# Kernel optimization log

Hardware: AMD Instinct MI355X
Metric: run time of the kernel (lower is better)

The kernel has to match this reference:

```python
import jax, jax.numpy as jnp
import numpy as np

NEG_SLOPE = 0.2


def gat_conv(h, src, dst, n_dst, W_src, W_dst, attn_l, attn_r, bias):
    # h: [N_src, F_in]; edges src->dst; dst nodes are a prefix of src nodes.
    H, D = attn_l.shape
    z_src = (h @ W_src).reshape(h.shape[0], H, D)          # [N_src, H, D]
    z_dst = (h[:n_dst] @ W_dst).reshape(n_dst, H, D)       # [N_dst, H, D]
    el = jnp.einsum('nhd,hd->nh', z_src, attn_l)           # [N_src, H]
    er = jnp.einsum('nhd,hd->nh', z_dst, attn_r)           # [N_dst, H]
    e = jax.nn.leaky_relu(el[src] + er[dst], NEG_SLOPE)    # [E, H]
    # numerically stable edge softmax over incoming edges of each dst node
    m = jax.ops.segment_max(e, dst, num_segments=n_dst)    # [N_dst, H]
    w = jnp.exp(e - m[dst])                                # [E, H]
    s = jax.ops.segment_sum(w, dst, num_segments=n_dst)    # [N_dst, H]
    alpha = w / s[dst]                                     # [E, H]
    msg = alpha[:, :, None] * z_src[src]                   # [E, H, D]
    out = jax.ops.segment_sum(msg, dst, num_segments=n_dst)
    return out + bias                                      # [N_dst, H, D]


def setup_inputs() -> dict:
    key = jax.random.key(0)
    ks = jax.random.split(key, 16)
    IN, HID, HEADS, NCLS = 256, 64, 4, 47
    N_SRC0, N_DST0, E0 = 200000, 50000, 500000
    N_DST1, E1 = 10000, 100000
    sc0 = 0.1
    inp = {
        'x': jax.random.normal(ks[0], (N_SRC0, IN), jnp.float32),
        'src0': jax.random.randint(ks[1], (E0,), 0, N_SRC0, jnp.int32),
        'dst0': jax.random.randint(ks[2], (E0,), 0, N_DST0, jnp.int32),
        'src1': jax.random.randint(ks[3], (E1,), 0, N_DST0, jnp.int32),
        'dst1': jax.random.randint(ks[4], (E1,), 0, N_DST1, jnp.int32),
        'num_dst0': N_DST0,
        'num_dst1': N_DST1,
        'W0_src': jax.random.normal(ks[5], (IN, HEADS * HID), jnp.float32) * sc0,
        'W0_dst': jax.random.normal(ks[6], (IN, HEADS * HID), jnp.float32) * sc0,
        'attn_l0': jax.random.normal(ks[7], (HEADS, HID), jnp.float32) * sc0,
        'attn_r0': jax.random.normal(ks[8], (HEADS, HID), jnp.float32) * sc0,
        'bias0': jnp.zeros((HEADS, HID), jnp.float32),
        'W1_src': jax.random.normal(ks[9], (HEADS * HID, HEADS * NCLS), jnp.float32) * sc0,
        'W1_dst': jax.random.normal(ks[10], (HEADS * HID, HEADS * NCLS), jnp.float32) * sc0,
        'attn_l1': jax.random.normal(ks[11], (HEADS, NCLS), jnp.float32) * sc0,
        'attn_r1': jax.random.normal(ks[12], (HEADS, NCLS), jnp.float32) * sc0,
        'bias1': jnp.zeros((HEADS, NCLS), jnp.float32),
    }
    return inp


def reference(x, src0, dst0, src1, dst1, num_dst0, num_dst1,
              W0_src, W0_dst, attn_l0, attn_r0, bias0,
              W1_src, W1_dst, attn_l1, attn_r1, bias1):
    # layer 0: GATConv + relu activation, flatten heads
    h = gat_conv(x, src0, dst0, num_dst0, W0_src, W0_dst, attn_l0, attn_r0, bias0)
    h = jax.nn.relu(h).reshape(num_dst0, -1)               # [N_dst0, H*HID]
    # layer 1: GATConv, no activation
    h = gat_conv(h, src1, dst1, num_dst1, W1_src, W1_dst, attn_l1, attn_r1, bias1)
    h = h.mean(axis=1)                                     # mean over heads -> [N_dst1, n_classes]
    return jax.nn.log_softmax(h, axis=-1)
```

## Files before the change

kernel.cpp:

```cpp
#include <hip/hip_runtime.h>
#include <math.h>

typedef _Float16 half8 __attribute__((ext_vector_type(8)));
typedef _Float16 half4 __attribute__((ext_vector_type(4)));
typedef float f32x4 __attribute__((ext_vector_type(4)));

constexpr int IN    = 256;
constexpr int NCLS  = 47;
constexpr int HD1   = 188;
constexpr float NEG_SLOPE = 0.2f;
constexpr int ND0 = 50000, ND1 = 10000;

static __device__ __forceinline__ float leaky(float x) {
    return x >= 0.f ? x : NEG_SLOPE * x;
}

__device__ __forceinline__ void gload16(const void* g, void* l) {
    __builtin_amdgcn_global_load_lds((const __attribute__((address_space(1))) void*)g,
                                     (__attribute__((address_space(3))) void*)l, 16, 0, 0);
}

__device__ __forceinline__ float red8(const float v[8], int lane) {
    const int b0 = lane & 1, b1 = (lane >> 1) & 1, b2 = (lane >> 2) & 1;
    float K[4];
#pragma unroll
    for (int i = 0; i < 4; ++i) {
        float send = b0 ? v[i] : v[i + 4];
        float r = __shfl_xor(send, 1);
        K[i] = (b0 ? v[i + 4] : v[i]) + r;
    }
    float L[2];
#pragma unroll
    for (int i = 0; i < 2; ++i) {
        float send = b1 ? K[i] : K[i + 2];
        float r = __shfl_xor(send, 2);
        L[i] = (b1 ? K[i + 2] : K[i]) + r;
    }
    float send = b2 ? L[0] : L[1];
    float r = __shfl_xor(send, 4);
    float Mv = (b2 ? L[1] : L[0]) + r;
    Mv += __shfl_xor(Mv, 8);
    Mv += __shfl_xor(Mv, 16);
    Mv += __shfl_xor(Mv, 32);
    return Mv;
}

__global__ __launch_bounds__(256) void prep_k(
        const float* __restrict__ W0s, const float* __restrict__ W1s,
        const float* __restrict__ W0d, const float* __restrict__ W1d,
        const float* __restrict__ al0, const float* __restrict__ ar0,
        const float* __restrict__ al1, const float* __restrict__ ar1,
        _Float16* __restrict__ B0p, _Float16* __restrict__ B1p,
        float* __restrict__ vl0T, float* __restrict__ vr0T,
        float* __restrict__ vl1T, float* __restrict__ vr1T) {
    int b = blockIdx.x, t = threadIdx.x;
    if (b < 256) {
        int id = b * 256 + t;
        int h = id >> 14, n = (id >> 8) & 63, k = id & 255;
        int dst = (h * 64 + n) * 256 + ((((k >> 3) ^ (n & 31)) & 31) << 3) + (k & 7);
        B0p[dst] = (_Float16)W0s[(size_t)k * 256 + h * 64 + n];
    } else if (b < 448) {
        int id = (b - 256) * 256 + t;
        int np = id >> 8, k = id & 255;
        int h = np / 48, n = np % 48;
        int dst = np * 256 + ((((k >> 3) ^ (n & 31)) & 31) << 3) + (k & 7);
        B1p[dst] = (n < NCLS) ? (_Float16)W1s[(size_t)k * HD1 + h * NCLS + n] : (_Float16)0.f;
    } else if (b == 448) {
        for (int i = t; i < 1024; i += 256) {
            int h = i >> 8, k = i & 255;
            float s = 0.f;
            for (int d = 0; d < 64; ++d)
                s += W0d[(size_t)k * 256 + h * 64 + d] * ar0[h * 64 + d];
            vr0T[h * 256 + k] = s;
        }
    } else if (b == 449) {
        for (int i = t; i < 1024; i += 256) {
            int h = i >> 8, k = i & 255;
            float s = 0.f;
            for (int d = 0; d < 64; ++d)
                s += W0s[(size_t)k * 256 + h * 64 + d] * al0[h * 64 + d];
            vl0T[h * 256 + k] = s;
        }
    } else if (b == 450) {
        for (int i = t; i < 1024; i += 256) {
            int h = i >> 8, k = i & 255;
            float s = 0.f;
            for (int d = 0; d < NCLS; ++d)
                s += W1s[(size_t)k * HD1 + h * NCLS + d] * al1[h * NCLS + d];
            vl1T[h * 256 + k] = s;
        }
    } else {
        for (int i = t; i < 1024; i += 256) {
            int h = i >> 8, k = i & 255;
            float s = 0.f;
            for (int d = 0; d < NCLS; ++d)
                s += W1d[(size_t)k * HD1 + h * NCLS + d] * ar1[h * NCLS + d];
            vr1T[h * 256 + k] = s;
        }
    }
}

template <bool F32IN, bool WRITE_XH>
__global__ __launch_bounds__(256) void lr_k(const void* __restrict__ Xv,
        const float* __restrict__ vlT, const float* __restrict__ vrT,
        _Float16* __restrict__ xh, float* __restrict__ el, float* __restrict__ er,
        int M, int Mr) {
    const int wv = threadIdx.x >> 6, lane = threadIdx.x & 63;
    const int gw0 = blockIdx.x * 4 + wv, NW = gridDim.x * 4;
    float vl[4][4], vr[4][4];
#pragma unroll
    for (int h = 0; h < 4; ++h) {
        float4 v = *(const float4*)(vlT + h * 256 + lane * 4);
        vl[h][0] = v.x; vl[h][1] = v.y; vl[h][2] = v.z; vl[h][3] = v.w;
        float4 u = *(const float4*)(vrT + h * 256 + lane * 4);
        vr[h][0] = u.x; vr[h][1] = u.y; vr[h][2] = u.z; vr[h][3] = u.w;
    }
    const int l7 = lane & 7;
    const int jj = ((l7 >> 1) & 1) * 2 + ((l7 >> 2) & 1);
    const bool isL = (l7 & 1) == 0;

    auto dorow = [&](int row) {
        float xa[4];
        if constexpr (F32IN) {
            float4 tv = *(const float4*)((const float*)Xv + (size_t)row * 256 + lane * 4);
            xa[0] = tv.x; xa[1] = tv.y; xa[2] = tv.z; xa[3] = tv.w;
            if constexpr (WRITE_XH) {
                half4 hv;
                hv[0] = (_Float16)tv.x; hv[1] = (_Float16)tv.y;
                hv[2] = (_Float16)tv.z; hv[3] = (_Float16)tv.w;
                *(half4*)(xh + (size_t)row * 256 + lane * 4) = hv;
            }
        } else {
            half4 tv = *(const half4*)((const _Float16*)Xv + (size_t)row * 256 + lane * 4);
            xa[0] = (float)tv[0]; xa[1] = (float)tv[1];
            xa[2] = (float)tv[2]; xa[3] = (float)tv[3];
        }
        float v8[8];
#pragma unroll
        for (int h = 0; h < 4; ++h) {
            v8[h]     = xa[0] * vl[h][0] + xa[1] * vl[h][1]
                      + xa[2] * vl[h][2] + xa[3] * vl[h][3];
            v8[h + 4] = xa[0] * vr[h][0] + xa[1] * vr[h][1]
                      + xa[2] * vr[h][2] + xa[3] * vr[h][3];
        }
        float Mv = red8(v8, lane);
        if (lane < 8) {
            if (isL) el[(size_t)row * 4 + jj] = Mv;
            else if (row < Mr) er[(size_t)row * 4 + jj] = Mv;
        }
    };

    int row = gw0;
    for (; row + NW < M; row += 2 * NW) { dorow(row); dorow(row + NW); }
    if (row < M) dorow(row);
}

__global__ __launch_bounds__(256) void aggx(const int* __restrict__ ssrc,
        const int* __restrict__ offs, int obase,
        const float* __restrict__ el, const float* __restrict__ er,
        const _Float16* __restrict__ srcF, _Float16* __restrict__ aggP,
        size_t PS, int nd) {
    int wv = threadIdx.x >> 6, lane = threadIdx.x & 63;
    int d = blockIdx.x * 4 + wv;
    if (d >= nd) return;
    int beg = offs[obase + d], end = offs[obase + d + 1];
    float4 er4 = *(const float4*)(er + (size_t)d * 4);
    float erv[4] = {er4.x, er4.y, er4.z, er4.w};
    float acc[4][4];
#pragma unroll
    for (int h = 0; h < 4; ++h)
#pragma unroll
        for (int e = 0; e < 4; ++e) acc[h][e] = 0.f;
    float S[4] = {0.f, 0.f, 0.f, 0.f};
    for (int j0 = beg; j0 < end; j0 += 64) {
        int nn = min(64, end - j0);
        int myidx = (lane < nn) ? ssrc[j0 + lane] : 0;
        int j = 0;
        for (; j + 4 <= nn; j += 4) {
            int s0 = __shfl(myidx, j),     s1 = __shfl(myidx, j + 1);
            int s2 = __shfl(myidx, j + 2), s3 = __shfl(myidx, j + 3);
            float4 e0 = *(const float4*)(el + (size_t)s0 * 4);
            float4 e1 = *(const float4*)(el + (size_t)s1 * 4);
            float4 e2 = *(const float4*)(el + (size_t)s2 * 4);
            float4 e3 = *(const float4*)(el + (size_t)s3 * 4);
            half4 x0 = *(const half4*)(srcF + (size_t)s0 * 256 + lane * 4);
            half4 x1 = *(const half4*)(srcF + (size_t)s1 * 256 + lane * 4);
            half4 x2 = *(const half4*)(srcF + (size_t)s2 * 256 + lane * 4);
            half4 x3 = *(const half4*)(srcF + (size_t)s3 * 256 + lane * 4);
            float ev0[4] = {e0.x, e0.y, e0.z, e0.w};
            float ev1[4] = {e1.x, e1.y, e1.z, e1.w};
            float ev2[4] = {e2.x, e2.y, e2.z, e2.w};
            float ev3[4] = {e3.x, e3.y, e3.z, e3.w};
            float w0[4], w1[4], w2[4], w3[4];
#pragma unroll
            for (int h = 0; h < 4; ++h) {
                w0[h] = __expf(leaky(ev0[h] + erv[h]));
                w1[h] = __expf(leaky(ev1[h] + erv[h]));
                w2[h] = __expf(leaky(ev2[h] + erv[h]));
                w3[h] = __expf(leaky(ev3[h] + erv[h]));
                S[h] += (w0[h] + w1[h]) + (w2[h] + w3[h]);
            }
            float f0[4] = {(float)x0[0], (float)x0[1], (float)x0[2], (float)x0[3]};
            float f1[4] = {(float)x1[0], (float)x1[1], (float)x1[2], (float)x1[3]};
            float f2[4] = {(float)x2[0], (float)x2[1], (float)x2[2], (float)x2[3]};
            float f3[4] = {(float)x3[0], (float)x3[1], (float)x3[2], (float)x3[3]};
#pragma unroll
            for (int h = 0; h < 4; ++h)
#pragma unroll
                for (int e = 0; e < 4; ++e)
                    acc[h][e] += (w0[h] * f0[e] + w1[h] * f1[e])
                               + (w2[h] * f2[e] + w3[h] * f3[e]);
        }
        for (; j < nn; ++j) {
            int s = __shfl(myidx, j);
            float4 ea = *(const float4*)(el + (size_t)s * 4);
            half4 xa = *(const half4*)(srcF + (size_t)s * 256 + lane * 4);
            float eav[4] = {ea.x, ea.y, ea.z, ea.w};
            float wa[4];
#pragma unroll
            for (int h = 0; h < 4; ++h) {
                wa[h] = __expf(leaky(eav[h] + erv[h]));
                S[h] += wa[h];
            }
            float fa[4] = {(float)xa[0], (float)xa[1], (float)xa[2], (float)xa[3]};
#pragma unroll
            for (int h = 0; h < 4; ++h)
#pragma unroll
                for (int e = 0; e < 4; ++e)
                    acc[h][e] += wa[h] * fa[e];
        }
    }
#pragma unroll
    for (int h = 0; h < 4; ++h) {
        float inv = S[h] > 0.f ? 1.f / S[h] : 0.f;
        half4 o;
#pragma unroll
        for (int e = 0; e < 4; ++e) o[e] = (_Float16)(acc[h][e] * inv);
        *(half4*)(aggP + (size_t)h * PS + (size_t)d * 256 + lane * 4) = o;
    }
}

template <int NCOLS, int CV, bool RELU, bool F32OUT, bool TRN>
__global__ __launch_bounds__(512, 2) void gemmp(const _Float16* __restrict__ Aplanes,
        size_t APS, const _Float16* __restrict__ Bplanes, const float* __restrict__ bias,
        void* __restrict__ Z, int zstride, int M, int ntiles) {
    constexpr int NCF = NCOLS / 16;
    __shared__ __align__(16) _Float16 Bs[NCOLS * 256];
    __shared__ __align__(16) _Float16 Ts[TRN ? 8 * 16 * 72 : 8];
    const int t = threadIdx.x, l = t & 63, w = t >> 6;
    const int lr = l & 15, lh = l >> 4;
    const int hplane = blockIdx.y;
    const _Float16* Ah  = Aplanes + (size_t)hplane * APS;
    const _Float16* BtS = Bplanes + (size_t)hplane * NCOLS * 256;
    _Float16* Tw = &Ts[TRN ? w * 16 * 72 : 0];

    constexpr int BI = NCOLS / 16;
#pragma unroll
    for (int it = 0; it < BI; ++it) {
        int c = it * 512 + t;
        gload16(BtS + c * 8, (char*)Bs + c * 16);
    }
    __syncthreads();

    float bcol[NCF];
#pragma unroll
    for (int cf = 0; cf < NCF; ++cf) {
        int col = cf * 16 + lr;
        bcol[cf] = (col < CV) ? bias[hplane * CV + col] : 0.f;
    }

    const int NW = gridDim.x * 8;
    const int gw = blockIdx.x * 8 + w;

    half8 p0[8], p1[8];

    auto issue = [&](int tile, half8 (&p)[8]) {
        int row = tile * 16 + lr; if (row >= M) row = M - 1;
        const _Float16* ap = Ah + (size_t)row * 256 + lh * 8;
#pragma unroll
        for (int ks = 0; ks < 8; ++ks) p[ks] = *(const half8*)(ap + ks * 32);
        __builtin_amdgcn_sched_barrier(0);
    };

    auto compute = [&](int tile, half8 (&p)[8]) {
        f32x4 acc[NCF];
#pragma unroll
        for (int cf = 0; cf < NCF; ++cf) {
            acc[cf][0] = 0.f; acc[cf][1] = 0.f; acc[cf][2] = 0.f; acc[cf][3] = 0.f;
        }
#pragma unroll
        for (int ks = 0; ks < 8; ++ks) {
#pragma unroll
            for (int cf = 0; cf < NCF; ++cf) {
                int colr = cf * 16 + lr;
                half8 bf = *(const half8*)&Bs[colr * 256 +
                                              ((((ks * 4 + lh) ^ (colr & 31)) & 31) << 3)];
                acc[cf] = __builtin_amdgcn_mfma_f32_16x16x32_f16(p[ks], bf, acc[cf], 0, 0, 0);
            }
        }
        if constexpr (TRN) {
#pragma unroll
            for (int cf = 0; cf < NCF; ++cf) {
#pragma unroll
                for (int r = 0; r < 4; ++r) {
                    float v = acc[cf][r] + bcol[cf];
                    if constexpr (RELU) v = fmaxf(v, 0.f);
                    Tw[(lh * 4 + r) * 72 + cf * 16 + lr] = (_Float16)v;
                }
            }
#pragma unroll
            for (int i = 0; i < 2; ++i) {
                int trow = i * 8 + (l >> 3);
                half8 hv = *(const half8*)&Tw[trow * 72 + (l & 7) * 8];
                int node = tile * 16 + trow;
                if (node < M)
                    *(half8*)((_Float16*)Z + (size_t)node * zstride + hplane * NCOLS
                              + (l & 7) * 8) = hv;
            }
        } else {
#pragma unroll
            for (int cf = 0; cf < NCF; ++cf) {
                int col = cf * 16 + lr;
                if (col < CV) {
#pragma unroll
                    for (int r = 0; r < 4; ++r) {
                        int row = tile * 16 + lh * 4 + r;
                        if (row < M) {
                            float v = acc[cf][r] + bcol[cf];
                            if constexpr (RELU) v = fmaxf(v, 0.f);
                            if constexpr (F32OUT)
                                ((float*)Z)[(size_t)row * zstride + hplane * CV + col] = v;
                            else
                                ((_Float16*)Z)[(size_t)row * zstride + hplane * CV + col] =
                                    (_Float16)v;
                        }
                    }
                }
            }
        }
    };

    if (gw < ntiles) issue(gw, p0);
    for (int tt = gw; tt < ntiles; tt += 2 * NW) {
        int t1 = tt + NW;
        if (t1 < ntiles) {
            issue(t1, p1);
            asm volatile("s_waitcnt vmcnt(8)" ::: "memory");
        } else {
            asm volatile("s_waitcnt vmcnt(0)" ::: "memory");
        }
        compute(tt, p0);
        if (t1 < ntiles) {
            int t2 = tt + 2 * NW;
            if (t2 < ntiles) {
                issue(t2, p0);
                asm volatile("s_waitcnt vmcnt(8)" ::: "memory");
            } else {
                asm volatile("s_waitcnt vmcnt(0)" ::: "memory");
            }
            compute(t1, p1);
        }
    }
}

__global__ void hist2_k(const int* __restrict__ dst0, int E0,
                        const int* __restrict__ dst1, int E1, int* __restrict__ counts) {
    int i = blockIdx.x * blockDim.x + threadIdx.x;
    if (i < E0) atomicAdd(&counts[dst0[i]], 1);
    else if (i < E0 + E1) atomicAdd(&counts[ND0 + dst1[i - E0]], 1);
}

__global__ __launch_bounds__(256) void scan1_k(const int* __restrict__ counts, int n,
                                               int* __restrict__ part) {
    __shared__ int ws[4];
    int i = blockIdx.x * 256 + threadIdx.x;
    int lane = threadIdx.x & 63, wv = threadIdx.x >> 6;
    int s = (i < n) ? counts[i] : 0;
#pragma unroll
    for (int off = 32; off; off >>= 1) s += __shfl_xor(s, off);
    if (lane == 0) ws[wv] = s;
    __syncthreads();
    if (threadIdx.x == 0) part[blockIdx.x] = ws[0] + ws[1] + ws[2] + ws[3];
}

__global__ __launch_bounds__(256) void scan2_k(int* __restrict__ part, int nb) {
    __shared__ int ws[4];
    int tid = threadIdx.x, lane = tid & 63, wv = tid >> 6;
    int v = (tid < nb) ? part[tid] : 0;
    int x = v;
#pragma unroll
    for (int off = 1; off < 64; off <<= 1) {
        int u = __shfl_up(x, off);
        if (lane >= off) x += u;
    }
    if (lane == 63) ws[wv] = x;
    __syncthreads();
    int base = 0;
    for (int k = 0; k < wv; ++k) base += ws[k];
    if (tid < nb) part[tid] = base + x - v;
}

__global__ __launch_bounds__(256) void scan3_k(const int* __restrict__ counts, int n,
        const int* __restrict__ part, int* __restrict__ offsets, int* __restrict__ cursor) {
    __shared__ int ws[4];
    int i = blockIdx.x * 256 + threadIdx.x;
    int lane = threadIdx.x & 63, wv = threadIdx.x >> 6;
    int v = (i < n) ? counts[i] : 0;
    int x = v;
#pragma unroll
    for (int off = 1; off < 64; off <<= 1) {
        int u = __shfl_up(x, off);
        if (lane >= off) x += u;
    }
    if (lane == 63) ws[wv] = x;
    __syncthreads();
    int base = part[blockIdx.x];
    for (int k = 0; k < wv; ++k) base += ws[k];
    int off_ = base + x - v;
    if (i < n) { offsets[i] = off_; cursor[i] = off_; }
    if (i == n - 1) offsets[n] = off_ + v;
}

__global__ void scatter2_k(const int* __restrict__ src0, const int* __restrict__ dst0, int E0,
                           const int* __restrict__ src1, const int* __restrict__ dst1, int E1,
                           int* __restrict__ cursor, int* __restrict__ ssrc) {
    int i = blockIdx.x * blockDim.x + threadIdx.x;
    if (i < E0) {
        int p = atomicAdd(&cursor[dst0[i]], 1);
        ssrc[p] = src0[i];
    } else if (i < E0 + E1) {
        int j = i - E0;
        int p = atomicAdd(&cursor[ND0 + dst1[j]], 1);
        ssrc[p] = src1[j];
    }
}

__global__ __launch_bounds__(256) void final_k(const float* __restrict__ o1,
        float* __restrict__ y, int n) {
    int wave = threadIdx.x >> 6, lane = threadIdx.x & 63;
    int node = blockIdx.x * 4 + wave;
    if (node >= n) return;
    const float* r = o1 + (size_t)node * HD1;
    float vv = 0.f, v = -INFINITY;
    if (lane < NCLS) {
        vv = 0.25f * (r[lane] + r[lane + NCLS] + r[lane + 2 * NCLS] + r[lane + 3 * NCLS]);
        v = vv;
    }
    float mx = v;
#pragma unroll
    for (int off = 32; off; off >>= 1) mx = fmaxf(mx, __shfl_xor(mx, off));
    float p = (lane < NCLS) ? __expf(vv - mx) : 0.f;
    float sum = p;
#pragma unroll
    for (int off = 32; off; off >>= 1) sum += __shfl_xor(sum, off);
    if (lane < NCLS) y[(size_t)node * NCLS + lane] = vv - mx - logf(sum);
}

extern "C" void kernel_launch(void* const* d_in, const int* in_sizes, int n_in,
                              void* d_out, int out_size, void* d_ws, size_t ws_size,
                              hipStream_t stream) {
    const float* x    = (const float*)d_in[0];
    const int*   src0 = (const int*)d_in[1];
    const int*   dst0 = (const int*)d_in[2];
    const int*   src1 = (const int*)d_in[3];
    const int*   dst1 = (const int*)d_in[4];
    const float* W0s  = (const float*)d_in[7];
    const float* W0d  = (const float*)d_in[8];
    const float* al0  = (const float*)d_in[9];
    const float* ar0  = (const float*)d_in[10];
    const float* b0   = (const float*)d_in[11];
    const float* W1s  = (const float*)d_in[12];
    const float* W1d  = (const float*)d_in[13];
    const float* al1  = (const float*)d_in[14];
    const float* ar1  = (const float*)d_in[15];
    const float* b1   = (const float*)d_in[16];
    const int E0 = in_sizes[1], E1 = in_sizes[3];
    const int NS0 = in_sizes[0] / IN;

    char* p = (char*)d_ws;
    auto take = [&](size_t bytes) {
        char* r = p;
        p += (bytes + 255) & ~(size_t)255;
        return r;
    };
    _Float16* xh    = (_Float16*)take((size_t)NS0 * 256 * 2);
    _Float16* aggP0 = (_Float16*)take((size_t)4 * ND0 * 256 * 2);
    _Float16* hbuf  = (_Float16*)take((size_t)ND0 * 256 * 2);
    _Float16* aggP1 = (_Float16*)take((size_t)4 * ND1 * 256 * 2);
    float*    o1    = (float*)take((size_t)ND1 * HD1 * 4);
    float*    el0   = (float*)take((size_t)NS0 * 4 * 4);
    float*    er0   = (float*)take((size_t)ND0 * 4 * 4);
    float*    el1   = (float*)take((size_t)ND0 * 4 * 4);
    float*    er1   = (float*)take((size_t)ND1 * 4 * 4);
    _Float16* B0p   = (_Float16*)take((size_t)4 * 64 * 256 * 2);
    _Float16* B1p   = (_Float16*)take((size_t)4 * 48 * 256 * 2);
    float*    vl0T  = (float*)take(4 * 256 * 4);
    float*    vr0T  = (float*)take(4 * 256 * 4);
    float*    vl1T  = (float*)take(4 * 256 * 4);
    float*    vr1T  = (float*)take(4 * 256 * 4);
    const int NDT = ND0 + ND1;
    int* counts = (int*)take((size_t)NDT * 4);
    int* offs   = (int*)take((size_t)(NDT + 1) * 4);
    int* cur    = (int*)take((size_t)NDT * 4);
    int* ss     = (int*)take((size_t)(E0 + E1) * 4);
    int* part   = (int*)take(256 * 4);

    const int NB = (NDT + 255) / 256;
    const int NT0 = (ND0 + 15) / 16, NT1 = (ND1 + 15) / 16;

    hipMemsetAsync(counts, 0, (size_t)NDT * 4, stream);

    prep_k<<<452, 256, 0, stream>>>(W0s, W1s, W0d, W1d, al0, ar0, al1, ar1,
                                    B0p, B1p, vl0T, vr0T, vl1T, vr1T);
    hist2_k<<<(E0 + E1 + 255) / 256, 256, 0, stream>>>(dst0, E0, dst1, E1, counts);
    scan1_k<<<NB, 256, 0, stream>>>(counts, NDT, part);
    scan2_k<<<1, 256, 0, stream>>>(part, NB);
    scan3_k<<<NB, 256, 0, stream>>>(counts, NDT, part, offs, cur);
    scatter2_k<<<(E0 + E1 + 255) / 256, 256, 0, stream>>>(src0, dst0, E0, src1, dst1, E1,
                                                          cur, ss);

    lr_k<true, true><<<1024, 256, 0, stream>>>((const void*)x, vl0T, vr0T,
                                               xh, el0, er0, NS0, ND0);
    aggx<<<(ND0 + 3) / 4, 256, 0, stream>>>(ss, offs, 0, el0, er0, xh,
                                            aggP0, (size_t)ND0 * 256, ND0);
    gemmp<64, 64, true, false, true><<<dim3(128, 4), 512, 0, stream>>>(
        aggP0, (size_t)ND0 * 256, B0p, b0, (void*)hbuf, 256, ND0, NT0);

    lr_k<false, false><<<512, 256, 0, stream>>>((const void*)hbuf, vl1T, vr1T,
                                                nullptr, el1, er1, ND0, ND1);
    aggx<<<(ND1 + 3) / 4, 256, 0, stream>>>(ss, offs, ND0, el1, er1, hbuf,
                                            aggP1, (size_t)ND1 * 256, ND1);
    gemmp<48, 47, false, true, false><<<dim3(32, 4), 512, 0, stream>>>(
        aggP1, (size_t)ND1 * 256, B1p, b1, (void*)o1, HD1, ND1, NT1);

    final_k<<<(ND1 + 3) / 4, 256, 0, stream>>>(o1, (float*)d_out, ND1);
}
```

Before: 310.4 us.

## Store aggregated features in MFMA fragment order and fuse histogram into prep

The aggregation kernel now writes its per-head output in a tiled layout that matches the GEMM's MFMA A-fragment order, so each GEMM lane loads contiguous 16-byte chunks at a fixed stride instead of row-strided reads. The row-clamp for partial tiles is dropped, which relies on node counts being multiples of 16. Separately, the histogram kernel is folded into the weight-prep kernel as extra blocks, removing one launch.

```diff
diff --git a/kernel.cpp b/kernel.cpp
--- a/kernel.cpp
+++ b/kernel.cpp
@@ -45,15 +45,23 @@
     return Mv;
 }
 
-__global__ __launch_bounds__(256) void prep_k(
+__global__ __launch_bounds__(256) void ph_k(
         const float* __restrict__ W0s, const float* __restrict__ W1s,
         const float* __restrict__ W0d, const float* __restrict__ W1d,
         const float* __restrict__ al0, const float* __restrict__ ar0,
         const float* __restrict__ al1, const float* __restrict__ ar1,
         _Float16* __restrict__ B0p, _Float16* __restrict__ B1p,
         float* __restrict__ vl0T, float* __restrict__ vr0T,
-        float* __restrict__ vl1T, float* __restrict__ vr1T) {
+        float* __restrict__ vl1T, float* __restrict__ vr1T,
+        const int* __restrict__ dst0, int E0,
+        const int* __restrict__ dst1, int E1, int* __restrict__ counts) {
     int b = blockIdx.x, t = threadIdx.x;
+    if (b >= 452) {
+        int i = (b - 452) * 256 + t;
+        if (i < E0) atomicAdd(&counts[dst0[i]], 1);
+        else if (i < E0 + E1) atomicAdd(&counts[ND0 + dst1[i - E0]], 1);
+        return;
+    }
     if (b < 256) {
         int id = b * 256 + t;
         int h = id >> 14, n = (id >> 8) & 63, k = id & 255;
@@ -230,13 +238,16 @@
                     acc[h][e] += wa[h] * fa[e];
         }
     }
+    const int tile = d >> 4, nr = d & 15;
+    const int ks = lane >> 3, lh2 = (lane >> 1) & 3, hf = lane & 1;
+    const size_t base = (size_t)tile * 4096 + ks * 512 + (lh2 * 16 + nr) * 8 + hf * 4;
 #pragma unroll
     for (int h = 0; h < 4; ++h) {
         float inv = S[h] > 0.f ? 1.f / S[h] : 0.f;
         half4 o;
 #pragma unroll
         for (int e = 0; e < 4; ++e) o[e] = (_Float16)(acc[h][e] * inv);
-        *(half4*)(aggP + (size_t)h * PS + (size_t)d * 256 + lane * 4) = o;
+        *(half4*)(aggP + (size_t)h * PS + base) = o;
     }
 }
 
@@ -275,10 +286,9 @@
     half8 p0[8], p1[8];
 
     auto issue = [&](int tile, half8 (&p)[8]) {
-        int row = tile * 16 + lr; if (row >= M) row = M - 1;
-        const _Float16* ap = Ah + (size_t)row * 256 + lh * 8;
-#pragma unroll
-        for (int ks = 0; ks < 8; ++ks) p[ks] = *(const half8*)(ap + ks * 32);
+        const _Float16* ap = Ah + (size_t)tile * 4096 + l * 8;
+#pragma unroll
+        for (int ks = 0; ks < 8; ++ks) p[ks] = *(const half8*)(ap + ks * 512);
         __builtin_amdgcn_sched_barrier(0);
     };
 
@@ -361,13 +371,6 @@
             compute(t1, p1);
         }
     }
-}
-
-__global__ void hist2_k(const int* __restrict__ dst0, int E0,
-                        const int* __restrict__ dst1, int E1, int* __restrict__ counts) {
-    int i = blockIdx.x * blockDim.x + threadIdx.x;
-    if (i < E0) atomicAdd(&counts[dst0[i]], 1);
-    else if (i < E0 + E1) atomicAdd(&counts[ND0 + dst1[i - E0]], 1);
 }
 
 __global__ __launch_bounds__(256) void scan1_k(const int* __restrict__ counts, int n,
@@ -483,10 +486,12 @@
         p += (bytes + 255) & ~(size_t)255;
         return r;
     };
+    const int NT0 = ND0 / 16, NT1 = ND1 / 16;
+    const size_t PS0 = (size_t)NT0 * 4096, PS1 = (size_t)NT1 * 4096;
     _Float16* xh    = (_Float16*)take((size_t)NS0 * 256 * 2);
-    _Float16* aggP0 = (_Float16*)take((size_t)4 * ND0 * 256 * 2);
+    _Float16* aggP0 = (_Float16*)take((size_t)4 * PS0 * 2);
     _Float16* hbuf  = (_Float16*)take((size_t)ND0 * 256 * 2);
-    _Float16* aggP1 = (_Float16*)take((size_t)4 * ND1 * 256 * 2);
+    _Float16* aggP1 = (_Float16*)take((size_t)4 * PS1 * 2);
     float*    o1    = (float*)take((size_t)ND1 * HD1 * 4);
     float*    el0   = (float*)take((size_t)NS0 * 4 * 4);
     float*    er0   = (float*)take((size_t)ND0 * 4 * 4);
@@ -506,13 +511,13 @@
     int* part   = (int*)take(256 * 4);
 
     const int NB = (NDT + 255) / 256;
-    const int NT0 = (ND0 + 15) / 16, NT1 = (ND1 + 15) / 16;
+    const int HB = (E0 + E1 + 255) / 256;
 
     hipMemsetAsync(counts, 0, (size_t)NDT * 4, stream);
 
-    prep_k<<<452, 256, 0, stream>>>(W0s, W1s, W0d, W1d, al0, ar0, al1, ar1,
-                                    B0p, B1p, vl0T, vr0T, vl1T, vr1T);
-    hist2_k<<<(E0 + E1 + 255) / 256, 256, 0, stream>>>(dst0, E0, dst1, E1, counts);
+    ph_k<<<452 + HB, 256, 0, stream>>>(W0s, W1s, W0d, W1d, al0, ar0, al1, ar1,
+                                       B0p, B1p, vl0T, vr0T, vl1T, vr1T,
+                                       dst0, E0, dst1, E1, counts);
     scan1_k<<<NB, 256, 0, stream>>>(counts, NDT, part);
     scan2_k<<<1, 256, 0, stream>>>(part, NB);
     scan3_k<<<NB, 256, 0, stream>>>(counts, NDT, part, offs, cur);
@@ -522,16 +527,16 @@
     lr_k<true, true><<<1024, 256, 0, stream>>>((const void*)x, vl0T, vr0T,
                                                xh, el0, er0, NS0, ND0);
     aggx<<<(ND0 + 3) / 4, 256, 0, stream>>>(ss, offs, 0, el0, er0, xh,
-                                            aggP0, (size_t)ND0 * 256, ND0);
+                                            aggP0, PS0, ND0);
     gemmp<64, 64, true, false, true><<<dim3(128, 4), 512, 0, stream>>>(
-        aggP0, (size_t)ND0 * 256, B0p, b0, (void*)hbuf, 256, ND0, NT0);
+        aggP0, PS0, B0p, b0, (void*)hbuf, 256, ND0, NT0);
 
     lr_k<false, false><<<512, 256, 0, stream>>>((const void*)hbuf, vl1T, vr1T,
                                                 nullptr, el1, er1, ND0, ND1);
     aggx<<<(ND1 + 3) / 4, 256, 0, stream>>>(ss, offs, ND0, el1, er1, hbuf,
-                                            aggP1, (size_t)ND1 * 256, ND1);
+                                            aggP1, PS1, ND1);
     gemmp<48, 47, false, true, false><<<dim3(32, 4), 512, 0, stream>>>(
-        aggP1, (size_t)ND1 * 256, B1p, b1, (void*)o1, HD1, ND1, NT1);
+        aggP1, PS1, B1p, b1, (void*)o1, HD1, ND1, NT1);
 
     final_k<<<(ND1 + 3) / 4, 256, 0, stream>>>(o1, (float*)d_out, ND1);
 }
```

After: 326.8 us. +5.3%, slower.
